# Kernel optimization log

Measured on AMD Instinct MI355X. Metric: run time of the kernel, lower is better.

## Reference

```python
import jax, jax.numpy as jnp
import numpy as np

STEPS = 32
LO, HI = 0.0, 1.0
BETA = 0.1
IMPULSE = float(1.0 / (abs(BETA) * np.sqrt(np.pi)))  # unused in fwd, kept for parity


def _cells(x):
    """Filtration values of all cells of the V-construction cubical complex.
    Vertices = pixels; edges = max of the 2 endpoint pixels; squares = max of 4 corners."""
    v = x                                                    # [B,C,H,W]   sign +1
    he = jnp.maximum(x[..., :, :-1], x[..., :, 1:])          # [B,C,H,W-1] sign -1
    ve = jnp.maximum(x[..., :-1, :], x[..., 1:, :])          # [B,C,H-1,W] sign -1
    sq = jnp.maximum(jnp.maximum(x[..., :-1, :-1], x[..., :-1, 1:]),
                     jnp.maximum(x[..., 1:, :-1], x[..., 1:, 1:]))  # [B,C,H-1,W-1] sign +1
    return v, he, ve, sq


def _ecc_forward(x):
    """Euler characteristic curve ECC(t) = #V(t) - #E(t) + #F(t) sampled on
    tseq = linspace(LO, HI, STEPS). Returns [B, C*STEPS] (flattened, matching nn.Flatten)."""
    B, C, H, W = x.shape
    BC = B * C
    tseq = jnp.linspace(LO, HI, STEPS, dtype=x.dtype)
    v, he, ve, sq = _cells(x)
    f = jnp.concatenate([v.reshape(BC, -1), he.reshape(BC, -1),
                         ve.reshape(BC, -1), sq.reshape(BC, -1)], axis=1)  # [BC, Ncells]
    signs = jnp.concatenate([
        jnp.ones(H * W, jnp.float32),
        -jnp.ones(H * (W - 1), jnp.float32),
        -jnp.ones((H - 1) * W, jnp.float32),
        jnp.ones((H - 1) * (W - 1), jnp.float32),
    ])
    # first threshold index j with tseq[j] >= f (cell is "alive" for all t >= idx)
    idx = jnp.searchsorted(tseq, f, side='left')            # [BC, Ncells], values in [0, STEPS]
    rows = jnp.arange(BC)[:, None]
    hist = jnp.zeros((BC, STEPS + 1), jnp.float32).at[rows, idx].add(signs[None, :])
    ecc = jnp.cumsum(hist[:, :STEPS], axis=1)               # [BC, STEPS]
    return ecc.reshape(B, C * STEPS)


def setup_inputs() -> dict:
    key = jax.random.key(0)
    x = jax.random.uniform(key, (64, 3, 224, 224), dtype=jnp.float32)
    return {"x": x}


def reference(x):
    return _ecc_forward(x)
```

## Files before the change

### kernel.cpp

```cpp
#include <hip/hip_runtime.h>
#include <hip/hip_bf16.h>


#define H 224
#define W 224
#define STEPS 32
#define NBINS 34
#define NCOL 64
#define BANDS 8
#define BAND_ROWS 28
#define SUB_ROWS 7
#define NTHR 256

__device__ __forceinline__ int bin_of(float f) {
    int i = (int)ceilf(f * 31.0f);
    return i > 31 ? 31 : i;
}

__global__ __launch_bounds__(NTHR, 6) void ecc_hist_kernel(
        const float* __restrict__ x, int* __restrict__ part)
{
    __shared__ int lh[NBINS * NCOL];
    __shared__ int partial[NTHR];

    const int tid = threadIdx.x;
    #pragma unroll
    for (int i = tid; i < NBINS * NCOL; i += NTHR) lh[i] = 0;
    __syncthreads();

    const int band = blockIdx.x & (BANDS - 1);
    const int img  = blockIdx.x / BANDS;
    const float* __restrict__ p = x + (size_t)img * (H * W);

    const int c = tid & 63;
    const int s = tid >> 6;

    if (c < 56) {
        const int  j0    = c << 2;
        const bool lastc = (c == 55);
        const int  jn    = lastc ? (j0 + 3) : (j0 + 4);
        const int  r0    = band * BAND_ROWS + s * SUB_ROWS;
        int* __restrict__ lhc = lh + c;

        float4 F = *(const float4*)(p + r0 * W + j0);
        float  fn = p[r0 * W + jn];
        int B0 = bin_of(F.x), B1 = bin_of(F.y), B2 = bin_of(F.z), B3 = bin_of(F.w);
        int Bn = lastc ? 33 : bin_of(fn);

        for (int r = r0; r < r0 + SUB_ROWS; ++r) {
            int C0, C1, C2, C3, Cn;
            if (r < H - 1) {
                float4 G = *(const float4*)(p + (r + 1) * W + j0);
                float  gn = p[(r + 1) * W + jn];
                C0 = bin_of(G.x); C1 = bin_of(G.y); C2 = bin_of(G.z); C3 = bin_of(G.w);
                Cn = lastc ? 33 : bin_of(gn);
            } else {
                C0 = C1 = C2 = C3 = 32; Cn = 32;
            }

            if (B1 > B0) { atomicAdd(&lhc[B0 << 6],  1); atomicAdd(&lhc[B1 << 6], -1); }
            if (B2 > B1) { atomicAdd(&lhc[B1 << 6],  1); atomicAdd(&lhc[B2 << 6], -1); }
            if (B3 > B2) { atomicAdd(&lhc[B2 << 6],  1); atomicAdd(&lhc[B3 << 6], -1); }
            if (Bn > B3) { atomicAdd(&lhc[B3 << 6],  1); atomicAdd(&lhc[Bn << 6], -1); }

            {
                int M0 = max(B0, C0), M1 = max(B1, C1), M2 = max(B2, C2),
                    M3 = max(B3, C3), Mn = max(Bn, Cn);
                if (M1 > M0) { atomicAdd(&lhc[M0 << 6], -1); atomicAdd(&lhc[M1 << 6], 1); }
                if (M2 > M1) { atomicAdd(&lhc[M1 << 6], -1); atomicAdd(&lhc[M2 << 6], 1); }
                if (M3 > M2) { atomicAdd(&lhc[M2 << 6], -1); atomicAdd(&lhc[M3 << 6], 1); }
                if (Mn > M3) { atomicAdd(&lhc[M3 << 6], -1); atomicAdd(&lhc[Mn << 6], 1); }
            }

            B0 = C0; B1 = C1; B2 = C2; B3 = C3; Bn = Cn;
        }
    }
    __syncthreads();

    const int b = tid >> 3;
    const int g = tid & 7;
    const int4* row = (const int4*)(lh + (b << 6) + (g << 3));
    int4 v0 = row[0], v1 = row[1];
    partial[tid] = v0.x + v0.y + v0.z + v0.w + v1.x + v1.y + v1.z + v1.w;
    __syncthreads();

    if (tid < 32) {
        const int4* pr = (const int4*)(partial + (tid << 3));
        int4 a0 = pr[0], a1 = pr[1];
        int s8 = a0.x + a0.y + a0.z + a0.w + a1.x + a1.y + a1.z + a1.w;
        part[(((img << 3) | band) << 5) + tid] = s8;
    }
}

__global__ __launch_bounds__(64) void ecc_cumsum_kernel(
        const int* __restrict__ part, float* __restrict__ out)
{
    const int img  = blockIdx.x;
    const int lane = threadIdx.x;
    if (lane < STEPS) {
        const int* pb = part + (img << 8) + lane;
        int s = 0;
        #pragma unroll
        for (int band = 0; band < BANDS; ++band) s += pb[band << 5];
        #pragma unroll
        for (int off = 1; off < STEPS; off <<= 1) {
            int v = __shfl_up(s, off);
            if (lane >= off) s += v;
        }
        out[img * STEPS + lane] = (float)s;
    }
}

extern "C" void kernel_launch(void* const* d_in, const int* in_sizes, int n_in,
                              void* d_out, int out_size, void* d_ws, size_t ws_size,
                              hipStream_t stream) {
    const float* x = (const float*)d_in[0];
    float* out = (float*)d_out;
    int* part = (int*)d_ws;

    const int nimg = in_sizes[0] / (H * W);

    dim3 grid1(nimg * BANDS);
    ecc_hist_kernel<<<grid1, NTHR, 0, stream>>>(x, part);

    ecc_cumsum_kernel<<<dim3(nimg), 64, 0, stream>>>(part, out);
}
```

Measured before the change: 79.15 us.

## Accumulate net per-cell Euler contributions to cut shared atomics

Each pixel now adds one combined signed contribution per row (vertex minus the edges it owns, and for the horizontal edge row, vertical edges minus squares), computed from left and right neighbour comparisons. This replaces pairs of paired atomics and is meant to reduce LDS atomic traffic. Neighbour bins are loaded with sentinel values at image borders, the bin clamp is removed so values of 1.0 map to bin 31 without a min, and the final bin reduction uses wavefront shuffles instead of a second shared-memory pass and barrier. The kernel now does an extra neighbour load per row, and correctness depends on the sentinel and bin-range handling being right.

New measurement: 79.41 us. No clear change (+0.3%).

```diff
diff --git a/kernel.cpp b/kernel.cpp
--- a/kernel.cpp
+++ b/kernel.cpp
@@ -5,7 +5,7 @@
 #define H 224
 #define W 224
 #define STEPS 32
-#define NBINS 34
+#define NBINS 33
 #define NCOL 64
 #define BANDS 8
 #define BAND_ROWS 28
@@ -13,18 +13,15 @@
 #define NTHR 256
 
 __device__ __forceinline__ int bin_of(float f) {
-    int i = (int)ceilf(f * 31.0f);
-    return i > 31 ? 31 : i;
+    return (int)ceilf(f * 31.0f);
 }
 
 __global__ __launch_bounds__(NTHR, 6) void ecc_hist_kernel(
         const float* __restrict__ x, int* __restrict__ part)
 {
     __shared__ int lh[NBINS * NCOL];
-    __shared__ int partial[NTHR];
 
     const int tid = threadIdx.x;
-    #pragma unroll
     for (int i = tid; i < NBINS * NCOL; i += NTHR) lh[i] = 0;
     __syncthreads();
 
@@ -36,60 +33,74 @@
     const int s = tid >> 6;
 
     if (c < 56) {
-        const int  j0    = c << 2;
-        const bool lastc = (c == 55);
-        const int  jn    = lastc ? (j0 + 3) : (j0 + 4);
-        const int  r0    = band * BAND_ROWS + s * SUB_ROWS;
+        const int  j0     = c << 2;
+        const bool lastc  = (c == 55);
+        const bool firstc = (c == 0);
+        const int  jn = lastc  ? (j0 + 3) : (j0 + 4);
+        const int  jp = firstc ? j0       : (j0 - 1);
+        const int  r0 = band * BAND_ROWS + s * SUB_ROWS;
         int* __restrict__ lhc = lh + c;
 
-        float4 F = *(const float4*)(p + r0 * W + j0);
-        float  fn = p[r0 * W + jn];
+        const float* __restrict__ row0 = p + r0 * W;
+        float4 F = *(const float4*)(row0 + j0);
         int B0 = bin_of(F.x), B1 = bin_of(F.y), B2 = bin_of(F.z), B3 = bin_of(F.w);
-        int Bn = lastc ? 33 : bin_of(fn);
+        int Bn = lastc  ? 0  : bin_of(row0[jn]);
+        int Bp = firstc ? 63 : bin_of(row0[jp]);
 
-        for (int r = r0; r < r0 + SUB_ROWS; ++r) {
-            int C0, C1, C2, C3, Cn;
-            if (r < H - 1) {
-                float4 G = *(const float4*)(p + (r + 1) * W + j0);
-                float  gn = p[(r + 1) * W + jn];
-                C0 = bin_of(G.x); C1 = bin_of(G.y); C2 = bin_of(G.z); C3 = bin_of(G.w);
-                Cn = lastc ? 33 : bin_of(gn);
-            } else {
-                C0 = C1 = C2 = C3 = 32; Cn = 32;
+        for (int k = 0; k < SUB_ROWS; ++k) {
+            const int r = r0 + k;
+
+            {
+                int dm = (B0 > Bp) ? 1 : 0;
+                int d0 = (B1 > B0) ? 1 : 0;
+                int d1 = (B2 > B1) ? 1 : 0;
+                int d2 = (B3 > B2) ? 1 : 0;
+                int d3 = (Bn > B3) ? 1 : 0;
+                int v0 = d0 - dm, v1 = d1 - d0, v2 = d2 - d1, v3 = d3 - d2;
+                if (v0) atomicAdd(&lhc[B0 << 6], v0);
+                if (v1) atomicAdd(&lhc[B1 << 6], v1);
+                if (v2) atomicAdd(&lhc[B2 << 6], v2);
+                if (v3) atomicAdd(&lhc[B3 << 6], v3);
             }
 
-            if (B1 > B0) { atomicAdd(&lhc[B0 << 6],  1); atomicAdd(&lhc[B1 << 6], -1); }
-            if (B2 > B1) { atomicAdd(&lhc[B1 << 6],  1); atomicAdd(&lhc[B2 << 6], -1); }
-            if (B3 > B2) { atomicAdd(&lhc[B2 << 6],  1); atomicAdd(&lhc[B3 << 6], -1); }
-            if (Bn > B3) { atomicAdd(&lhc[B3 << 6],  1); atomicAdd(&lhc[Bn << 6], -1); }
+            if (r < H - 1) {
+                const float* __restrict__ row1 = p + (r + 1) * W;
+                float4 G = *(const float4*)(row1 + j0);
+                int C0 = bin_of(G.x), C1 = bin_of(G.y),
+                    C2 = bin_of(G.z), C3 = bin_of(G.w);
+                int Cn = lastc  ? 0  : bin_of(row1[jn]);
+                int Cp = firstc ? 63 : bin_of(row1[jp]);
 
-            {
-                int M0 = max(B0, C0), M1 = max(B1, C1), M2 = max(B2, C2),
-                    M3 = max(B3, C3), Mn = max(Bn, Cn);
-                if (M1 > M0) { atomicAdd(&lhc[M0 << 6], -1); atomicAdd(&lhc[M1 << 6], 1); }
-                if (M2 > M1) { atomicAdd(&lhc[M1 << 6], -1); atomicAdd(&lhc[M2 << 6], 1); }
-                if (M3 > M2) { atomicAdd(&lhc[M2 << 6], -1); atomicAdd(&lhc[M3 << 6], 1); }
-                if (Mn > M3) { atomicAdd(&lhc[M3 << 6], -1); atomicAdd(&lhc[Mn << 6], 1); }
+                int M0 = max(B0, C0), M1 = max(B1, C1),
+                    M2 = max(B2, C2), M3 = max(B3, C3);
+                int Mn = max(Bn, Cn), Mp = max(Bp, Cp);
+                int em = (M0 > Mp) ? 1 : 0;
+                int e0 = (M1 > M0) ? 1 : 0;
+                int e1 = (M2 > M1) ? 1 : 0;
+                int e2 = (M3 > M2) ? 1 : 0;
+                int e3 = (Mn > M3) ? 1 : 0;
+                int w0 = em - e0, w1 = e0 - e1, w2 = e1 - e2, w3 = e2 - e3;
+                if (w0) atomicAdd(&lhc[M0 << 6], w0);
+                if (w1) atomicAdd(&lhc[M1 << 6], w1);
+                if (w2) atomicAdd(&lhc[M2 << 6], w2);
+                if (w3) atomicAdd(&lhc[M3 << 6], w3);
+
+                B0 = C0; B1 = C1; B2 = C2; B3 = C3; Bn = Cn; Bp = Cp;
             }
-
-            B0 = C0; B1 = C1; B2 = C2; B3 = C3; Bn = Cn;
         }
     }
     __syncthreads();
 
     const int b = tid >> 3;
     const int g = tid & 7;
-    const int4* row = (const int4*)(lh + (b << 6) + (g << 3));
-    int4 v0 = row[0], v1 = row[1];
-    partial[tid] = v0.x + v0.y + v0.z + v0.w + v1.x + v1.y + v1.z + v1.w;
-    __syncthreads();
-
-    if (tid < 32) {
-        const int4* pr = (const int4*)(partial + (tid << 3));
-        int4 a0 = pr[0], a1 = pr[1];
-        int s8 = a0.x + a0.y + a0.z + a0.w + a1.x + a1.y + a1.z + a1.w;
-        part[(((img << 3) | band) << 5) + tid] = s8;
-    }
+    const int4* rowp = (const int4*)(lh + (b << 6) + (g << 3));
+    int4 u0 = rowp[0], u1 = rowp[1];
+    int sum = u0.x + u0.y + u0.z + u0.w + u1.x + u1.y + u1.z + u1.w;
+    sum += __shfl_xor(sum, 1);
+    sum += __shfl_xor(sum, 2);
+    sum += __shfl_xor(sum, 4);
+    if (g == 0)
+        part[(((img << 3) | band) << 5) + b] = sum;
 }
 
 __global__ __launch_bounds__(64) void ecc_cumsum_kernel(
```
